# Kernel optimization log

Hardware: AMD Instinct MI355X
Metric: run time of the kernel (lower is better)

## Reference

```python
import jax, jax.numpy as jnp
import numpy as np

N, E = 50000, 800000
NODE_DIM, EDGE_DIM, HID = 128, 32, 128
NEG_SLOPE = 0.2


def _init(key, shape, fan_in):
    # glorot-ish init for weights
    return jax.random.normal(key, shape, dtype=jnp.float32) * (1.0 / np.sqrt(fan_in))


def setup_inputs() -> dict:
    key = jax.random.key(0)
    ks = jax.random.split(key, 20)
    x = jax.random.normal(ks[0], (N, NODE_DIM), dtype=jnp.float32)
    edge_index = jax.random.randint(ks[1], (2, E), 0, N, dtype=jnp.int64)
    edge_attr = jax.random.normal(ks[2], (E, EDGE_DIM), dtype=jnp.float32)
    params = {
        'W_emb': _init(ks[3], (NODE_DIM, HID), NODE_DIM),
        'b_emb': jnp.zeros((HID,), jnp.float32),
        # conv1 (GATv2Conv, heads=1)
        'Wl1': _init(ks[4], (HID, HID), HID), 'bl1': jnp.zeros((HID,), jnp.float32),
        'Wr1': _init(ks[5], (HID, HID), HID),
        'We1': _init(ks[6], (EDGE_DIM, HID), EDGE_DIM),
        'att1': _init(ks[7], (HID,), HID),
        'bo1': jnp.zeros((HID,), jnp.float32),
        # conv2
        'Wl2': _init(ks[8], (HID, HID), HID), 'bl2': jnp.zeros((HID,), jnp.float32),
        'Wr2': _init(ks[9], (HID, HID), HID),
        'We2': _init(ks[10], (EDGE_DIM, HID), EDGE_DIM),
        'att2': _init(ks[11], (HID,), HID),
        'bo2': jnp.zeros((HID,), jnp.float32),
    }
    return {'x': x, 'edge_index': edge_index, 'edge_attr': edge_attr, **params}


def _gatv2(x, src, dst, edge_attr, Wl, bl, Wr, We, att, bo, n_nodes):
    """PyG GATv2Conv (heads=1, add_self_loops=True, fill_value='mean')."""
    xl = x @ Wl + bl          # [N, H] source transform
    xr = x @ Wr               # [N, H] target transform
    # --- add self loops; self-loop edge_attr = mean of incoming edge_attr ---
    ones = jnp.ones((src.shape[0],), x.dtype)
    deg = jax.ops.segment_sum(ones, dst, num_segments=n_nodes)
    loop_attr = jax.ops.segment_sum(edge_attr, dst, num_segments=n_nodes) \
        / jnp.maximum(deg, 1.0)[:, None]
    loops = jnp.arange(n_nodes, dtype=src.dtype)
    src2 = jnp.concatenate([src, loops])
    dst2 = jnp.concatenate([dst, loops])
    ea2 = jnp.concatenate([edge_attr, loop_attr], axis=0)
    # --- per-edge attention (GATv2: leaky_relu AFTER the sum, score via att) ---
    xl_j = xl[src2]                                  # [E', H]
    msg = xl_j + xr[dst2] + ea2 @ We                 # [E', H]
    logits = jax.nn.leaky_relu(msg, NEG_SLOPE) @ att  # [E']
    # --- softmax over incoming edges per target node ---
    m = jax.ops.segment_max(logits, dst2, num_segments=n_nodes)
    ez = jnp.exp(logits - m[dst2])
    denom = jax.ops.segment_sum(ez, dst2, num_segments=n_nodes)
    alpha = ez / denom[dst2]                         # [E']
    # --- scatter-add aggregation ---
    out = jax.ops.segment_sum(alpha[:, None] * xl_j, dst2, num_segments=n_nodes)
    return out + bo


def reference(x, edge_index, edge_attr, W_emb, b_emb,
              Wl1, bl1, Wr1, We1, att1, bo1,
              Wl2, bl2, Wr2, We2, att2, bo2):
    src, dst = edge_index[0], edge_index[1]
    n = x.shape[0]
    h = x @ W_emb + b_emb
    h = jax.nn.silu(_gatv2(h, src, dst, edge_attr, Wl1, bl1, Wr1, We1, att1, bo1, n))
    h = jax.nn.silu(_gatv2(h, src, dst, edge_attr, Wl2, bl2, Wr2, We2, att2, bo2, n))
    return h
```

## Files before the change

### kernel.cpp

```cpp
#include <hip/hip_runtime.h>
#include <hip/hip_bf16.h>
#include <math.h>


#define HIP_N 50000
#define HIP_E 800000
#define HIP_H 128
#define HIP_ED 32
#define NEG_SLOPE 0.2f
#define RESCALE_THR_LOG2 11.5416f
#define LINM 3125
#define SCATB ((HIP_E + 255) / 256)
#define INV_LN2 1.4426950408889634f

typedef __fp16 h2 __attribute__((ext_vector_type(2)));
typedef _Float16 half8 __attribute__((ext_vector_type(8)));
typedef float f32x4 __attribute__((ext_vector_type(4)));

__device__ __forceinline__ h2 u2h(unsigned int u) {
    union { unsigned int u; h2 h; } c; c.u = u; return c.h;
}
__device__ __forceinline__ unsigned int pkh(float a, float b) {
    union { h2 h; unsigned int u; } c;
    c.h = __builtin_amdgcn_cvt_pkrtz(a, b);
    return c.u;
}
__device__ __forceinline__ float2 h2f(unsigned int u) {
    h2 h = u2h(u);
    return make_float2((float)h.x, (float)h.y);
}
__device__ __forceinline__ half8 u4h8(uint4 u) {
    union { uint4 u; half8 h; } c; c.u = u; return c.h;
}

__device__ __forceinline__ int fetch_idx(const int* __restrict__ ei, int is32, long long pos) {
    return is32 ? ei[pos] : ei[2 * pos];
}

__device__ __forceinline__ int wave_is32(const int* __restrict__ ei, int e) {
    int probe = (e < HIP_E) ? ei[2 * (long long)e + 1] : 0;
    return __any(probe != 0);
}

#define PREP_NB (420 + (HIP_N + 127) / 128)

__global__ __launch_bounds__(128) void k_prep(
    const float* __restrict__ Wemb, const float* __restrict__ bemb,
    const float* __restrict__ Wl1, const float* __restrict__ bl1,
    const float* __restrict__ Wr1,
    const float* __restrict__ Wl2, const float* __restrict__ bl2,
    const float* __restrict__ Wr2,
    const float* __restrict__ We1, const float* __restrict__ We2,
    unsigned short* __restrict__ Wt1, unsigned short* __restrict__ Wt2,
    float* __restrict__ b1, float* __restrict__ b2,
    unsigned int* __restrict__ Wepk1, unsigned int* __restrict__ Wepk2,
    int* __restrict__ deg) {
    int b = blockIdx.x, t = threadIdx.x;
    if (b < 256) {
        int r = b & 127;
        const float* W = (b < 128) ? Wl1 : Wr1;
        int nofs = (b < 128) ? 0 : 128;
        float acc = 0.f;
        for (int k = 0; k < 128; ++k) acc += Wemb[r * 128 + k] * W[k * 128 + t];
        union { __fp16 h; unsigned short s; } cv;
        cv.h = (__fp16)acc;
        Wt1[(size_t)(nofs + t) * 128 + r] = cv.s;
    } else if (b == 256) {
        float acc = bl1[t];
        for (int k = 0; k < 128; ++k) acc += bemb[k] * Wl1[k * 128 + t];
        b1[t] = acc;
    } else if (b == 257) {
        float acc = 0.f;
        for (int k = 0; k < 128; ++k) acc += bemb[k] * Wr1[k * 128 + t];
        b1[128 + t] = acc;
    } else if (b == 258) {
        b2[t] = bl2[t];
    } else if (b == 259) {
        b2[128 + t] = 0.f;
    } else if (b < 388) {
        int k = b - 260;
        float vl = Wl2[k * 128 + t], vr = Wr2[k * 128 + t];
        union { __fp16 h; unsigned short s; } c1, c2;
        c1.h = (__fp16)vl; c2.h = (__fp16)vr;
        Wt2[(size_t)t * 128 + k] = c1.s;
        Wt2[(size_t)(128 + t) * 128 + k] = c2.s;
    } else if (b < 420) {
        int idx = (b - 388) * 128 + t;
        const float* We = (idx < 2048) ? We1 : We2;
        unsigned int* P = (idx < 2048) ? Wepk1 : Wepk2;
        int r = idx & 2047;
        int d2 = r >> 7, rem = r & 127;
        int j = rem >> 6, tt = rem & 63;
        int col = 2 * tt + j;
        P[r] = pkh(We[(2 * d2) * 128 + col], We[(2 * d2 + 1) * 128 + col]);
    } else {
        int i = (b - 420) * 128 + t;
        if (i < HIP_N) deg[i] = 0;
    }
}

__global__ void k_hist(const int* __restrict__ ei, int* __restrict__ deg) {
    int e = blockIdx.x * blockDim.x + threadIdx.x;
    int is32 = wave_is32(ei, e);
    if (e < HIP_E) {
        int d = fetch_idx(ei, is32, (long long)HIP_E + e);
        atomicAdd(&deg[d], 1);
    }
}

#define SCAN_TILE 1024
#define SCAN_NB ((HIP_N + SCAN_TILE - 1) / SCAN_TILE)

__global__ __launch_bounds__(256) void k_scan1(const int* __restrict__ deg,
                                               int* __restrict__ bsums) {
    __shared__ int ws[4];
    int b = blockIdx.x, t = threadIdx.x;
    int base = b * SCAN_TILE;
    int v = 0;
#pragma unroll
    for (int j = 0; j < 4; ++j) {
        int i = base + t + 256 * j;
        if (i < HIP_N) v += deg[i];
    }
#pragma unroll
    for (int off = 32; off > 0; off >>= 1) v += __shfl_xor(v, off);
    int lane = t & 63, wid = t >> 6;
    if (lane == 0) ws[wid] = v;
    __syncthreads();
    if (t == 0) bsums[b] = ws[0] + ws[1] + ws[2] + ws[3];
}

__global__ __launch_bounds__(1024) void k_scan3(const int* __restrict__ deg,
                                                const int* __restrict__ bsums,
                                                int* __restrict__ offs,
                                                int* __restrict__ cursor) {
    __shared__ int wsum[16];
    __shared__ int bbase_sh;
    int b = blockIdx.x, t = threadIdx.x;
    int i = b * SCAN_TILE + t;
    int lane = t & 63, wid = t >> 6;
    if (wid == 0) {
        int v = (lane < SCAN_NB && lane < b) ? bsums[lane] : 0;
#pragma unroll
        for (int off = 32; off > 0; off >>= 1) v += __shfl_xor(v, off);
        if (lane == 0) bbase_sh = v;
    }
    int v = (i < HIP_N) ? deg[i] : 0;
    int incl = v;
#pragma unroll
    for (int off = 1; off < 64; off <<= 1) {
        int u = __shfl_up(incl, off);
        if (lane >= off) incl += u;
    }
    if (lane == 63) wsum[wid] = incl;
    __syncthreads();
    if (wid == 0 && lane < 16) {
        int w = wsum[lane];
#pragma unroll
        for (int off = 1; off < 16; off <<= 1) {
            int u = __shfl_up(w, off);
            if (lane >= off) w += u;
        }
        wsum[lane] = w;
    }
    __syncthreads();
    int baseadd = bbase_sh + (wid > 0 ? wsum[wid - 1] : 0);
    int excl = baseadd + incl - v;
    if (i < HIP_N) {
        offs[i] = excl;
        cursor[i] = excl;
        if (i == HIP_N - 1) offs[HIP_N] = excl + v;
    }
}

template <bool AHALF>
__device__ __forceinline__ void linm_body(const float* __restrict__ Af,
                                          const unsigned int* __restrict__ Ah,
                                          const unsigned short* __restrict__ Wt,
                                          const float* __restrict__ bias,
                                          unsigned int* __restrict__ xlh,
                                          unsigned int* __restrict__ xrh, int blk) {
    int tid = threadIdx.x;
    int wid = tid >> 6, l = tid & 63;
    int li = l & 15, lk = l >> 4;
    int rowA = blk * 16 + li;

    f32x4 acc0 = {0.f, 0.f, 0.f, 0.f};
    f32x4 acc1 = {0.f, 0.f, 0.f, 0.f};
    f32x4 acc2 = {0.f, 0.f, 0.f, 0.f};
    f32x4 acc3 = {0.f, 0.f, 0.f, 0.f};

#pragma unroll
    for (int ks = 0; ks < 4; ++ks) {
        int kb = ks * 32 + lk * 8;
        half8 afrag;
        if (AHALF) {
            afrag = u4h8(*(const uint4*)(Ah + (size_t)rowA * 64 + (kb >> 1)));
        } else {
            const float4* ap = (const float4*)(Af + (size_t)rowA * 128 + kb);
            float4 a0 = ap[0], a1 = ap[1];
            afrag = u4h8(make_uint4(pkh(a0.x, a0.y), pkh(a0.z, a0.w),
                                    pkh(a1.x, a1.y), pkh(a1.z, a1.w)));
        }
        int nbase = wid * 64 + li;
        half8 b0 = u4h8(*(const uint4*)(Wt + (size_t)(nbase +  0) * 128 + kb));
        half8 b1 = u4h8(*(const uint4*)(Wt + (size_t)(nbase + 16) * 128 + kb));
        half8 b2 = u4h8(*(const uint4*)(Wt + (size_t)(nbase + 32) * 128 + kb));
        half8 b3 = u4h8(*(const uint4*)(Wt + (size_t)(nbase + 48) * 128 + kb));
        acc0 = __builtin_amdgcn_mfma_f32_16x16x32_f16(afrag, b0, acc0, 0, 0, 0);
        acc1 = __builtin_amdgcn_mfma_f32_16x16x32_f16(afrag, b1, acc1, 0, 0, 0);
        acc2 = __builtin_amdgcn_mfma_f32_16x16x32_f16(afrag, b2, acc2, 0, 0, 0);
        acc3 = __builtin_amdgcn_mfma_f32_16x16x32_f16(afrag, b3, acc3, 0, 0, 0);
    }

    bool even = !(l & 1);
#pragma unroll
    for (int nt = 0; nt < 4; ++nt) {
        f32x4 a = (nt == 0) ? acc0 : (nt == 1) ? acc1 : (nt == 2) ? acc2 : acc3;
        int n = wid * 64 + nt * 16 + li;
        float bb = bias[n];
        unsigned int* outp = (n < 128) ? xlh : xrh;
        int nn = n & 127;
#pragma unroll
        for (int r = 0; r < 4; ++r) {
            int rowg = blk * 16 + lk * 4 + r;
            float v = a[r] + bb;
            float v1 = __shfl_down(v, 1);
            if (even) outp[(size_t)rowg * 64 + (nn >> 1)] = pkh(v, v1);
        }
    }
}

__device__ __forceinline__ void scatter_body(const int* __restrict__ ei, int is32,
                                             int* __restrict__ cursor,
                                             int* __restrict__ e_src,
                                             const float* __restrict__ ea,
                                             unsigned int* __restrict__ ea_h, int e) {
    if (e < HIP_E) {
        int s = fetch_idx(ei, is32, e);
        int d = fetch_idx(ei, is32, (long long)HIP_E + e);
        int pos = atomicAdd(&cursor[d], 1);
        e_src[pos] = s;
        const float4* src4 = (const float4*)(ea + (size_t)e * HIP_ED);
        float4 s0 = src4[0], s1 = src4[1], s2 = src4[2], s3 = src4[3];
        float4 s4 = src4[4], s5 = src4[5], s6 = src4[6], s7 = src4[7];
        uint4* dst = (uint4*)(ea_h + (size_t)pos * 16);
        dst[0] = make_uint4(pkh(s0.x, s0.y), pkh(s0.z, s0.w),
                            pkh(s1.x, s1.y), pkh(s1.z, s1.w));
        dst[1] = make_uint4(pkh(s2.x, s2.y), pkh(s2.z, s2.w),
                            pkh(s3.x, s3.y), pkh(s3.z, s3.w));
        dst[2] = make_uint4(pkh(s4.x, s4.y), pkh(s4.z, s4.w),
                            pkh(s5.x, s5.y), pkh(s5.z, s5.w));
        dst[3] = make_uint4(pkh(s6.x, s6.y), pkh(s6.z, s6.w),
                            pkh(s7.x, s7.y), pkh(s7.z, s7.w));
    }
}

__global__ __launch_bounds__(256) void k_fat1(
    const float* __restrict__ x, const unsigned short* __restrict__ Wt1,
    const float* __restrict__ b1,
    unsigned int* __restrict__ xlh, unsigned int* __restrict__ xrh,
    const int* __restrict__ ei,
    int* __restrict__ cursor, int* __restrict__ e_src,
    const float* __restrict__ ea, unsigned int* __restrict__ ea_h) {
    if (blockIdx.x < LINM) {
        linm_body<false>(x, nullptr, Wt1, b1, xlh, xrh, blockIdx.x);
    } else {
        int e = (blockIdx.x - LINM) * 256 + threadIdx.x;
        int is32 = wave_is32(ei, e);
        scatter_body(ei, is32, cursor, e_src, ea, ea_h, e);
    }
}

__global__ __launch_bounds__(256) void k_linm(const unsigned int* __restrict__ hh,
                                              const unsigned short* __restrict__ Wt,
                                              const float* __restrict__ bias,
                                              unsigned int* __restrict__ xlh,
                                              unsigned int* __restrict__ xrh) {
    linm_body<true>(nullptr, hh, Wt, bias, xlh, xrh, blockIdx.x);
}

template <int OUTH>
__global__ __launch_bounds__(64) void k_node_fused(
    const int* __restrict__ offs, const int* __restrict__ e_src,
    const unsigned int* __restrict__ ea_h,
    const unsigned int* __restrict__ Wepk, const float* __restrict__ att,
    const unsigned int* __restrict__ xlh, const unsigned int* __restrict__ xrh,
    const float* __restrict__ bo,
    unsigned int* __restrict__ houth, float* __restrict__ houtf) {
    int i = blockIdx.x;
    int t = threadIdx.x;

    h2 wx00 = u2h(Wepk[ 0*128 + t]),      wy00 = u2h(Wepk[ 0*128 + 64 + t]);
    h2 wx01 = u2h(Wepk[ 1*128 + t]),      wy01 = u2h(Wepk[ 1*128 + 64 + t]);
    h2 wx02 = u2h(Wepk[ 2*128 + t]),      wy02 = u2h(Wepk[ 2*128 + 64 + t]);
    h2 wx03 = u2h(Wepk[ 3*128 + t]),      wy03 = u2h(Wepk[ 3*128 + 64 + t]);
    h2 wx04 = u2h(Wepk[ 4*128 + t]),      wy04 = u2h(Wepk[ 4*128 + 64 + t]);
    h2 wx05 = u2h(Wepk[ 5*128 + t]),      wy05 = u2h(Wepk[ 5*128 + 64 + t]);
    h2 wx06 = u2h(Wepk[ 6*128 + t]),      wy06 = u2h(Wepk[ 6*128 + 64 + t]);
    h2 wx07 = u2h(Wepk[ 7*128 + t]),      wy07 = u2h(Wepk[ 7*128 + 64 + t]);
    h2 wx08 = u2h(Wepk[ 8*128 + t]),      wy08 = u2h(Wepk[ 8*128 + 64 + t]);
    h2 wx09 = u2h(Wepk[ 9*128 + t]),      wy09 = u2h(Wepk[ 9*128 + 64 + t]);
    h2 wx10 = u2h(Wepk[10*128 + t]),      wy10 = u2h(Wepk[10*128 + 64 + t]);
    h2 wx11 = u2h(Wepk[11*128 + t]),      wy11 = u2h(Wepk[11*128 + 64 + t]);
    h2 wx12 = u2h(Wepk[12*128 + t]),      wy12 = u2h(Wepk[12*128 + 64 + t]);
    h2 wx13 = u2h(Wepk[13*128 + t]),      wy13 = u2h(Wepk[13*128 + 64 + t]);
    h2 wx14 = u2h(Wepk[14*128 + t]),      wy14 = u2h(Wepk[14*128 + 64 + t]);
    h2 wx15 = u2h(Wepk[15*128 + t]),      wy15 = u2h(Wepk[15*128 + 64 + t]);

    float2 attv = ((const float2*)att)[t];
    attv.x *= INV_LN2; attv.y *= INV_LN2;
    float2 bov  = ((const float2*)bo)[t];
    float2 xri  = h2f(xrh[(size_t)i * 64 + t]);
    float2 xli  = h2f(xlh[(size_t)i * 64 + t]);

    float m = -1e30f;
    float denom = 0.f;
    float accx = 0.f, accy = 0.f;
    float epsx = 0.f, epsy = 0.f;

    int o0 = offs[i], o1 = offs[i + 1];
    int cnt = o1 - o0;
    int pairs = cnt >> 1;

#define DOTP(EX, EY, U, K)                                            \
    EX = __builtin_amdgcn_fdot2(u2h(U), wx##K, EX, false);            \
    EY = __builtin_amdgcn_fdot2(u2h(U), wy##K, EY, false);

#define EPROJ(EX, EY, P)                                              \
    {                                                                 \
        uint4 q0 = ((const uint4*)(P))[0];                            \
        uint4 q1 = ((const uint4*)(P))[1];                            \
        uint4 q2 = ((const uint4*)(P))[2];                            \
        uint4 q3 = ((const uint4*)(P))[3];                            \
        DOTP(EX, EY, q0.x, 00) DOTP(EX, EY, q0.y, 01)                 \
        DOTP(EX, EY, q0.z, 02) DOTP(EX, EY, q0.w, 03)                 \
        DOTP(EX, EY, q1.x, 04) DOTP(EX, EY, q1.y, 05)                 \
        DOTP(EX, EY, q1.z, 06) DOTP(EX, EY, q1.w, 07)                 \
        DOTP(EX, EY, q2.x, 08) DOTP(EX, EY, q2.y, 09)                 \
        DOTP(EX, EY, q2.z, 10) DOTP(EX, EY, q2.w, 11)                 \
        DOTP(EX, EY, q3.x, 12) DOTP(EX, EY, q3.y, 13)                 \
        DOTP(EX, EY, q3.z, 14) DOTP(EX, EY, q3.w, 15)                 \
    }

    unsigned int uA = 0, uB = 0;
    if (pairs > 0) {
        int s0 = e_src[o0];
        int s1 = e_src[o0 + 1];
        uA = xlh[(size_t)s0 * 64 + t];
        uB = xlh[(size_t)s1 * 64 + t];
    }

    for (int pp = 0; pp < pairs; ++pp) {
        int e = o0 + 2 * pp;
        float2 x0 = h2f(uA), x1 = h2f(uB);
        if (pp + 1 < pairs) {
            int s0 = e_src[e + 2];
            int s1 = e_src[e + 3];
            uA = xlh[(size_t)s0 * 64 + t];
            uB = xlh[(size_t)s1 * 64 + t];
        }
        const unsigned int* er = ea_h + (size_t)e * 16;
        float ex0 = 0.f, ey0 = 0.f, ex1 = 0.f, ey1 = 0.f;
        EPROJ(ex0, ey0, er)
        EPROJ(ex1, ey1, er + 16)
        epsx += ex0 + ex1; epsy += ey0 + ey1;
        float vx0 = x0.x + xri.x + ex0, vy0 = x0.y + xri.y + ey0;
        float vx1 = x1.x + xri.x + ex1, vy1 = x1.y + xri.y + ey1;
        vx0 = fmaxf(vx0, NEG_SLOPE * vx0);
        vy0 = fmaxf(vy0, NEG_SLOPE * vy0);
        vx1 = fmaxf(vx1, NEG_SLOPE * vx1);
        vy1 = fmaxf(vy1, NEG_SLOPE * vy1);
        float p0 = vx0 * attv.x + vy0 * attv.y;
        float p1 = vx1 * attv.x + vy1 * attv.y;
#pragma unroll
        for (int off = 32; off > 0; off >>= 1) {
            p0 += __shfl_xor(p0, off);
            p1 += __shfl_xor(p1, off);
        }
        float pm = fmaxf(p0, p1);
        if (pm > m + RESCALE_THR_LOG2) {
            float sc = exp2f(m - pm);
            accx *= sc; accy *= sc; denom *= sc;
            m = pm;
        }
        float wA = exp2f(p0 - m);
        float wB = exp2f(p1 - m);
        accx += wA * x0.x + wB * x1.x;
        accy += wA * x0.y + wB * x1.y;
        denom += wA + wB;
    }

    if (cnt & 1) {
        int e = o1 - 1;
        int s = e_src[e];
        float2 x0 = h2f(xlh[(size_t)s * 64 + t]);
        const unsigned int* er = ea_h + (size_t)e * 16;
        float ex = 0.f, ey = 0.f;
        EPROJ(ex, ey, er)
        epsx += ex; epsy += ey;
        float vx = x0.x + xri.x + ex;
        float vy = x0.y + xri.y + ey;
        vx = fmaxf(vx, NEG_SLOPE * vx);
        vy = fmaxf(vy, NEG_SLOPE * vy);
        float p = vx * attv.x + vy * attv.y;
#pragma unroll
        for (int off = 32; off > 0; off >>= 1) p += __shfl_xor(p, off);
        if (p > m + RESCALE_THR_LOG2) {
            float sc = exp2f(m - p);
            accx *= sc; accy *= sc; denom *= sc;
            m = p;
        }
        float w = exp2f(p - m);
        accx += w * x0.x;
        accy += w * x0.y;
        denom += w;
    }
#undef EPROJ
#undef DOTP

    float invdeg = 1.f / fmaxf((float)cnt, 1.f);
    float sx = xli.x + xri.x + epsx * invdeg;
    float sy = xli.y + xri.y + epsy * invdeg;
    sx = fmaxf(sx, NEG_SLOPE * sx);
    sy = fmaxf(sy, NEG_SLOPE * sy);
    float ps = sx * attv.x + sy * attv.y;
#pragma unroll
    for (int off = 32; off > 0; off >>= 1) ps += __shfl_xor(ps, off);

    float mm = fmaxf(m, ps);
    float wf = exp2f(m - mm);
    float ws = exp2f(ps - mm);
    denom = denom * wf + ws;
    accx = accx * wf + ws * xli.x;
    accy = accy * wf + ws * xli.y;

    float ox = accx / denom + bov.x;
    float oy = accy / denom + bov.y;
    float sox = ox / (1.f + __expf(-ox));
    float soy = oy / (1.f + __expf(-oy));
    if (OUTH) {
        houth[(size_t)i * 64 + t] = pkh(sox, soy);
    } else {
        float2 o; o.x = sox; o.y = soy;
        ((float2*)(houtf + (size_t)i * HIP_H))[t] = o;
    }
}

extern "C" void kernel_launch(void* const* d_in, const int* in_sizes, int n_in,
                              void* d_out, int out_size, void* d_ws, size_t ws_size,
                              hipStream_t stream) {
    const float* x      = (const float*)d_in[0];
    const int*   ei     = (const int*)d_in[1];
    const float* ea     = (const float*)d_in[2];
    const float* W_emb  = (const float*)d_in[3];
    const float* b_emb  = (const float*)d_in[4];
    const float* Wl1    = (const float*)d_in[5];
    const float* bl1    = (const float*)d_in[6];
    const float* Wr1    = (const float*)d_in[7];
    const float* We1    = (const float*)d_in[8];
    const float* att1   = (const float*)d_in[9];
    const float* bo1    = (const float*)d_in[10];
    const float* Wl2    = (const float*)d_in[11];
    const float* bl2    = (const float*)d_in[12];
    const float* Wr2    = (const float*)d_in[13];
    const float* We2    = (const float*)d_in[14];
    const float* att2   = (const float*)d_in[15];
    const float* bo2    = (const float*)d_in[16];
    float* out = (float*)d_out;

    char* p = (char*)d_ws;
    auto carve = [&](size_t bytes) {
        void* q = (void*)p;
        p += (bytes + 255) / 256 * 256;
        return q;
    };
    unsigned int* hh  = (unsigned int*)carve((size_t)HIP_N * 64 * 4);
    unsigned int* xlh = (unsigned int*)carve((size_t)HIP_N * 64 * 4);
    unsigned int* xrh = (unsigned int*)carve((size_t)HIP_N * 64 * 4);
    unsigned int* ea_h = (unsigned int*)carve((size_t)HIP_E * 16 * 4);
    int*   deg      = (int*)carve((size_t)HIP_N * 4);
    int*   offs     = (int*)carve((size_t)(HIP_N + 1) * 4);
    int*   cursor   = (int*)carve((size_t)HIP_N * 4);
    int*   e_src    = (int*)carve((size_t)HIP_E * 4);
    int*   bsums    = (int*)carve((size_t)SCAN_NB * 4);
    unsigned int* Wepk1 = (unsigned int*)carve(2048 * 4);
    unsigned int* Wepk2 = (unsigned int*)carve(2048 * 4);
    unsigned short* Wt1 = (unsigned short*)carve(256 * 128 * 2);
    unsigned short* Wt2 = (unsigned short*)carve(256 * 128 * 2);
    float* b1       = (float*)carve(256 * 4);
    float* b2       = (float*)carve(256 * 4);

    k_prep<<<PREP_NB, 128, 0, stream>>>(W_emb, b_emb, Wl1, bl1, Wr1,
                                        Wl2, bl2, Wr2, We1, We2,
                                        Wt1, Wt2, b1, b2,
                                        Wepk1, Wepk2, deg);

    k_hist<<<(HIP_E + 255) / 256, 256, 0, stream>>>(ei, deg);
    k_scan1<<<SCAN_NB, 256, 0, stream>>>(deg, bsums);
    k_scan3<<<SCAN_NB, 1024, 0, stream>>>(deg, bsums, offs, cursor);

    k_fat1<<<LINM + SCATB, 256, 0, stream>>>(x, Wt1, b1, xlh, xrh,
                                             ei, cursor, e_src, ea, ea_h);

    k_node_fused<1><<<HIP_N, 64, 0, stream>>>(offs, e_src, ea_h, Wepk1, att1,
                                              xlh, xrh, bo1, hh, nullptr);
    k_linm<<<LINM, 256, 0, stream>>>(hh, Wt2, b2, xlh, xrh);
    k_node_fused<0><<<HIP_N, 64, 0, stream>>>(offs, e_src, ea_h, Wepk2, att2,
                                              xlh, xrh, bo2, nullptr, out);
}
```

Baseline: 436.5 us.

## Compute per-edge attribute projection with MFMA in node attention kernel

The per-node attention kernel now processes 16 incoming edges per iteration and computes the edge-attribute projection with 16x16x32 f16 MFMA instructions instead of per-lane fdot2 chains. The hidden feature layout is permuted so each lane owns 8 interleaved channels; the linear kernels' epilogues, the layer-2 weight packing and the att/bias vectors are reordered to match. This targets the ALU-bound edge projection and widens gathers to 16-byte loads. The cost is padding waste for low-degree nodes, extra cross-lane reductions, and a more fragile layout contract between kernels.

```diff
diff --git a/kernel.cpp b/kernel.cpp
--- a/kernel.cpp
+++ b/kernel.cpp
@@ -25,10 +25,8 @@
     c.h = __builtin_amdgcn_cvt_pkrtz(a, b);
     return c.u;
 }
-__device__ __forceinline__ float2 h2f(unsigned int u) {
-    h2 h = u2h(u);
-    return make_float2((float)h.x, (float)h.y);
-}
+__device__ __forceinline__ float hlo(unsigned int u) { return (float)u2h(u).x; }
+__device__ __forceinline__ float hhi(unsigned int u) { return (float)u2h(u).y; }
 __device__ __forceinline__ half8 u4h8(uint4 u) {
     union { uint4 u; half8 h; } c; c.u = u; return c.h;
 }
@@ -42,7 +40,7 @@
     return __any(probe != 0);
 }
 
-#define PREP_NB (420 + (HIP_N + 127) / 128)
+#define PREP_NB (400 + (HIP_N + 127) / 128)
 
 __global__ __launch_bounds__(128) void k_prep(
     const float* __restrict__ Wemb, const float* __restrict__ bemb,
@@ -51,9 +49,13 @@
     const float* __restrict__ Wl2, const float* __restrict__ bl2,
     const float* __restrict__ Wr2,
     const float* __restrict__ We1, const float* __restrict__ We2,
+    const float* __restrict__ att1, const float* __restrict__ bo1,
+    const float* __restrict__ att2, const float* __restrict__ bo2,
     unsigned short* __restrict__ Wt1, unsigned short* __restrict__ Wt2,
     float* __restrict__ b1, float* __restrict__ b2,
-    unsigned int* __restrict__ Wepk1, unsigned int* __restrict__ Wepk2,
+    uint4* __restrict__ WemB1, uint4* __restrict__ WemB2,
+    float* __restrict__ attp1, float* __restrict__ bop1,
+    float* __restrict__ attp2, float* __restrict__ bop2,
     int* __restrict__ deg) {
     int b = blockIdx.x, t = threadIdx.x;
     if (b < 256) {
@@ -78,23 +80,36 @@
     } else if (b == 259) {
         b2[128 + t] = 0.f;
     } else if (b < 388) {
-        int k = b - 260;
-        float vl = Wl2[k * 128 + t], vr = Wr2[k * 128 + t];
+        int pk = b - 260;
+        int d = (pk >> 3) + ((pk & 7) << 4);
+        float vl = Wl2[d * 128 + t], vr = Wr2[d * 128 + t];
         union { __fp16 h; unsigned short s; } c1, c2;
         c1.h = (__fp16)vl; c2.h = (__fp16)vr;
-        Wt2[(size_t)t * 128 + k] = c1.s;
-        Wt2[(size_t)(128 + t) * 128 + k] = c2.s;
-    } else if (b < 420) {
+        Wt2[(size_t)t * 128 + pk] = c1.s;
+        Wt2[(size_t)(128 + t) * 128 + pk] = c2.s;
+    } else if (b < 396) {
         int idx = (b - 388) * 128 + t;
-        const float* We = (idx < 2048) ? We1 : We2;
-        unsigned int* P = (idx < 2048) ? Wepk1 : Wepk2;
-        int r = idx & 2047;
-        int d2 = r >> 7, rem = r & 127;
-        int j = rem >> 6, tt = rem & 63;
-        int col = 2 * tt + j;
-        P[r] = pkh(We[(2 * d2) * 128 + col], We[(2 * d2 + 1) * 128 + col]);
+        int layer = idx >> 9, rem = idx & 511;
+        int n = rem >> 6, ll = rem & 63;
+        int col = 16 * n + (ll & 15);
+        int kb = (ll >> 4) * 8;
+        const float* We = layer ? We2 : We1;
+        uint4 v = make_uint4(
+            pkh(We[(kb + 0) * 128 + col], We[(kb + 1) * 128 + col]),
+            pkh(We[(kb + 2) * 128 + col], We[(kb + 3) * 128 + col]),
+            pkh(We[(kb + 4) * 128 + col], We[(kb + 5) * 128 + col]),
+            pkh(We[(kb + 6) * 128 + col], We[(kb + 7) * 128 + col]));
+        (layer ? WemB2 : WemB1)[rem] = v;
+    } else if (b < 400) {
+        int which = b - 396;
+        int li = t >> 3, q = t & 7;
+        int src = li + 16 * q;
+        if (which == 0)      attp1[t] = att1[src] * INV_LN2;
+        else if (which == 1) bop1[t]  = bo1[src];
+        else if (which == 2) attp2[t] = att2[src] * INV_LN2;
+        else                 bop2[t]  = bo2[src];
     } else {
-        int i = (b - 420) * 128 + t;
+        int i = (b - 400) * 128 + t;
         if (i < HIP_N) deg[i] = 0;
     }
 }
@@ -213,21 +228,21 @@
         acc3 = __builtin_amdgcn_mfma_f32_16x16x32_f16(afrag, b3, acc3, 0, 0, 0);
     }
 
-    bool even = !(l & 1);
-#pragma unroll
-    for (int nt = 0; nt < 4; ++nt) {
-        f32x4 a = (nt == 0) ? acc0 : (nt == 1) ? acc1 : (nt == 2) ? acc2 : acc3;
-        int n = wid * 64 + nt * 16 + li;
-        float bb = bias[n];
-        unsigned int* outp = (n < 128) ? xlh : xrh;
-        int nn = n & 127;
-#pragma unroll
-        for (int r = 0; r < 4; ++r) {
-            int rowg = blk * 16 + lk * 4 + r;
-            float v = a[r] + bb;
-            float v1 = __shfl_down(v, 1);
-            if (even) outp[(size_t)rowg * 64 + (nn >> 1)] = pkh(v, v1);
-        }
+    unsigned int* outp = (wid < 2) ? xlh : xrh;
+    int wsel = wid & 1;
+    float bb0 = bias[wid * 64 +  0 + li];
+    float bb1 = bias[wid * 64 + 16 + li];
+    float bb2 = bias[wid * 64 + 32 + li];
+    float bb3 = bias[wid * 64 + 48 + li];
+#pragma unroll
+    for (int r = 0; r < 4; ++r) {
+        int rowg = blk * 16 + lk * 4 + r;
+        float v0 = acc0[r] + bb0;
+        float v1 = acc1[r] + bb1;
+        float v2 = acc2[r] + bb2;
+        float v3 = acc3[r] + bb3;
+        uint2 st = make_uint2(pkh(v0, v1), pkh(v2, v3));
+        *(uint2*)(outp + (size_t)rowg * 64 + li * 4 + wsel * 2) = st;
     }
 }
 
@@ -281,169 +296,174 @@
 }
 
 template <int OUTH>
-__global__ __launch_bounds__(64) void k_node_fused(
+__global__ __launch_bounds__(64) void k_node_mfma(
     const int* __restrict__ offs, const int* __restrict__ e_src,
     const unsigned int* __restrict__ ea_h,
-    const unsigned int* __restrict__ Wepk, const float* __restrict__ att,
+    const uint4* __restrict__ WemB, const float* __restrict__ att_p,
     const unsigned int* __restrict__ xlh, const unsigned int* __restrict__ xrh,
-    const float* __restrict__ bo,
+    const float* __restrict__ bo_p,
     unsigned int* __restrict__ houth, float* __restrict__ houtf) {
     int i = blockIdx.x;
-    int t = threadIdx.x;
-
-    h2 wx00 = u2h(Wepk[ 0*128 + t]),      wy00 = u2h(Wepk[ 0*128 + 64 + t]);
-    h2 wx01 = u2h(Wepk[ 1*128 + t]),      wy01 = u2h(Wepk[ 1*128 + 64 + t]);
-    h2 wx02 = u2h(Wepk[ 2*128 + t]),      wy02 = u2h(Wepk[ 2*128 + 64 + t]);
-    h2 wx03 = u2h(Wepk[ 3*128 + t]),      wy03 = u2h(Wepk[ 3*128 + 64 + t]);
-    h2 wx04 = u2h(Wepk[ 4*128 + t]),      wy04 = u2h(Wepk[ 4*128 + 64 + t]);
-    h2 wx05 = u2h(Wepk[ 5*128 + t]),      wy05 = u2h(Wepk[ 5*128 + 64 + t]);
-    h2 wx06 = u2h(Wepk[ 6*128 + t]),      wy06 = u2h(Wepk[ 6*128 + 64 + t]);
-    h2 wx07 = u2h(Wepk[ 7*128 + t]),      wy07 = u2h(Wepk[ 7*128 + 64 + t]);
-    h2 wx08 = u2h(Wepk[ 8*128 + t]),      wy08 = u2h(Wepk[ 8*128 + 64 + t]);
-    h2 wx09 = u2h(Wepk[ 9*128 + t]),      wy09 = u2h(Wepk[ 9*128 + 64 + t]);
-    h2 wx10 = u2h(Wepk[10*128 + t]),      wy10 = u2h(Wepk[10*128 + 64 + t]);
-    h2 wx11 = u2h(Wepk[11*128 + t]),      wy11 = u2h(Wepk[11*128 + 64 + t]);
-    h2 wx12 = u2h(Wepk[12*128 + t]),      wy12 = u2h(Wepk[12*128 + 64 + t]);
-    h2 wx13 = u2h(Wepk[13*128 + t]),      wy13 = u2h(Wepk[13*128 + 64 + t]);
-    h2 wx14 = u2h(Wepk[14*128 + t]),      wy14 = u2h(Wepk[14*128 + 64 + t]);
-    h2 wx15 = u2h(Wepk[15*128 + t]),      wy15 = u2h(Wepk[15*128 + 64 + t]);
-
-    float2 attv = ((const float2*)att)[t];
-    attv.x *= INV_LN2; attv.y *= INV_LN2;
-    float2 bov  = ((const float2*)bo)[t];
-    float2 xri  = h2f(xrh[(size_t)i * 64 + t]);
-    float2 xli  = h2f(xlh[(size_t)i * 64 + t]);
-
-    float m = -1e30f;
-    float denom = 0.f;
-    float accx = 0.f, accy = 0.f;
-    float epsx = 0.f, epsy = 0.f;
+    int l = threadIdx.x, li = l & 15, lk = l >> 4;
+
+    float attv[8], xriv[8];
+    {
+        const float4* ap = (const float4*)(att_p + li * 8);
+        float4 q0 = ap[0], q1 = ap[1];
+        attv[0]=q0.x; attv[1]=q0.y; attv[2]=q0.z; attv[3]=q0.w;
+        attv[4]=q1.x; attv[5]=q1.y; attv[6]=q1.z; attv[7]=q1.w;
+        uint4 xr4 = *(const uint4*)(xrh + (size_t)i * 64 + li * 4);
+        xriv[0]=hlo(xr4.x); xriv[1]=hhi(xr4.x); xriv[2]=hlo(xr4.y); xriv[3]=hhi(xr4.y);
+        xriv[4]=hlo(xr4.z); xriv[5]=hhi(xr4.z); xriv[6]=hlo(xr4.w); xriv[7]=hhi(xr4.w);
+    }
 
     int o0 = offs[i], o1 = offs[i + 1];
     int cnt = o1 - o0;
-    int pairs = cnt >> 1;
-
-#define DOTP(EX, EY, U, K)                                            \
-    EX = __builtin_amdgcn_fdot2(u2h(U), wx##K, EX, false);            \
-    EY = __builtin_amdgcn_fdot2(u2h(U), wy##K, EY, false);
-
-#define EPROJ(EX, EY, P)                                              \
-    {                                                                 \
-        uint4 q0 = ((const uint4*)(P))[0];                            \
-        uint4 q1 = ((const uint4*)(P))[1];                            \
-        uint4 q2 = ((const uint4*)(P))[2];                            \
-        uint4 q3 = ((const uint4*)(P))[3];                            \
-        DOTP(EX, EY, q0.x, 00) DOTP(EX, EY, q0.y, 01)                 \
-        DOTP(EX, EY, q0.z, 02) DOTP(EX, EY, q0.w, 03)                 \
-        DOTP(EX, EY, q1.x, 04) DOTP(EX, EY, q1.y, 05)                 \
-        DOTP(EX, EY, q1.z, 06) DOTP(EX, EY, q1.w, 07)                 \
-        DOTP(EX, EY, q2.x, 08) DOTP(EX, EY, q2.y, 09)                 \
-        DOTP(EX, EY, q2.z, 10) DOTP(EX, EY, q2.w, 11)                 \
-        DOTP(EX, EY, q3.x, 12) DOTP(EX, EY, q3.y, 13)                 \
-        DOTP(EX, EY, q3.z, 14) DOTP(EX, EY, q3.w, 15)                 \
-    }
-
-    unsigned int uA = 0, uB = 0;
-    if (pairs > 0) {
-        int s0 = e_src[o0];
-        int s1 = e_src[o0 + 1];
-        uA = xlh[(size_t)s0 * 64 + t];
-        uB = xlh[(size_t)s1 * 64 + t];
-    }
-
-    for (int pp = 0; pp < pairs; ++pp) {
-        int e = o0 + 2 * pp;
-        float2 x0 = h2f(uA), x1 = h2f(uB);
-        if (pp + 1 < pairs) {
-            int s0 = e_src[e + 2];
-            int s1 = e_src[e + 3];
-            uA = xlh[(size_t)s0 * 64 + t];
-            uB = xlh[(size_t)s1 * 64 + t];
-        }
-        const unsigned int* er = ea_h + (size_t)e * 16;
-        float ex0 = 0.f, ey0 = 0.f, ex1 = 0.f, ey1 = 0.f;
-        EPROJ(ex0, ey0, er)
-        EPROJ(ex1, ey1, er + 16)
-        epsx += ex0 + ex1; epsy += ey0 + ey1;
-        float vx0 = x0.x + xri.x + ex0, vy0 = x0.y + xri.y + ey0;
-        float vx1 = x1.x + xri.x + ex1, vy1 = x1.y + xri.y + ey1;
-        vx0 = fmaxf(vx0, NEG_SLOPE * vx0);
-        vy0 = fmaxf(vy0, NEG_SLOPE * vy0);
-        vx1 = fmaxf(vx1, NEG_SLOPE * vx1);
-        vy1 = fmaxf(vy1, NEG_SLOPE * vy1);
-        float p0 = vx0 * attv.x + vy0 * attv.y;
-        float p1 = vx1 * attv.x + vy1 * attv.y;
-#pragma unroll
-        for (int off = 32; off > 0; off >>= 1) {
-            p0 += __shfl_xor(p0, off);
-            p1 += __shfl_xor(p1, off);
-        }
-        float pm = fmaxf(p0, p1);
+
+    float m = -1e30f, denom = 0.f;
+    float acc[8] = {0,0,0,0,0,0,0,0};
+    float eps[8] = {0,0,0,0,0,0,0,0};
+
+    for (int base = o0; base < o1; base += 16) {
+        int ea_e = base + li;
+        uint4 au = (ea_e < o1) ? *(const uint4*)(ea_h + (size_t)ea_e * 16 + lk * 4)
+                               : make_uint4(0, 0, 0, 0);
+        half8 afrag = u4h8(au);
+
+        int sv[4]; int val[4]; uint4 xlu[4];
+#pragma unroll
+        for (int r = 0; r < 4; ++r) {
+            int idx = base + lk * 4 + r;
+            val[r] = idx < o1;
+            sv[r] = val[r] ? e_src[idx] : 0;
+        }
+#pragma unroll
+        for (int r = 0; r < 4; ++r)
+            xlu[r] = *(const uint4*)(xlh + (size_t)sv[r] * 64 + li * 4);
+
+        float p[4] = {0.f, 0.f, 0.f, 0.f};
+#pragma unroll
+        for (int pass = 0; pass < 2; ++pass) {
+            const uint4* wb = WemB + pass * 256 + l;
+            half8 bf0 = u4h8(wb[0]);
+            half8 bf1 = u4h8(wb[64]);
+            half8 bf2 = u4h8(wb[128]);
+            half8 bf3 = u4h8(wb[192]);
+            f32x4 c0 = {0,0,0,0}, c1 = {0,0,0,0}, c2 = {0,0,0,0}, c3 = {0,0,0,0};
+            c0 = __builtin_amdgcn_mfma_f32_16x16x32_f16(afrag, bf0, c0, 0, 0, 0);
+            c1 = __builtin_amdgcn_mfma_f32_16x16x32_f16(afrag, bf1, c1, 0, 0, 0);
+            c2 = __builtin_amdgcn_mfma_f32_16x16x32_f16(afrag, bf2, c2, 0, 0, 0);
+            c3 = __builtin_amdgcn_mfma_f32_16x16x32_f16(afrag, bf3, c3, 0, 0, 0);
+#pragma unroll
+            for (int nn = 0; nn < 4; ++nn) {
+                int n = pass * 4 + nn;
+                f32x4 C = (nn == 0) ? c0 : (nn == 1) ? c1 : (nn == 2) ? c2 : c3;
+                float av = attv[n], xr_ = xriv[n];
+#pragma unroll
+                for (int r = 0; r < 4; ++r) {
+                    unsigned int dw = ((const unsigned int*)&xlu[r])[n >> 1];
+                    float xv = (n & 1) ? hhi(dw) : hlo(dw);
+                    float v = xv + xr_ + C[r];
+                    v = fmaxf(v, NEG_SLOPE * v);
+                    p[r] += v * av;
+                }
+                eps[n] += C[0] + C[1] + C[2] + C[3];
+            }
+        }
+#pragma unroll
+        for (int off = 1; off <= 8; off <<= 1) {
+            p[0] += __shfl_xor(p[0], off);
+            p[1] += __shfl_xor(p[1], off);
+            p[2] += __shfl_xor(p[2], off);
+            p[3] += __shfl_xor(p[3], off);
+        }
+#pragma unroll
+        for (int r = 0; r < 4; ++r) if (!val[r]) p[r] = -1e30f;
+        float pm = fmaxf(fmaxf(p[0], p[1]), fmaxf(p[2], p[3]));
+        pm = fmaxf(pm, __shfl_xor(pm, 16));
+        pm = fmaxf(pm, __shfl_xor(pm, 32));
         if (pm > m + RESCALE_THR_LOG2) {
             float sc = exp2f(m - pm);
-            accx *= sc; accy *= sc; denom *= sc;
+#pragma unroll
+            for (int q = 0; q < 8; ++q) acc[q] *= sc;
+            denom *= sc;
             m = pm;
         }
-        float wA = exp2f(p0 - m);
-        float wB = exp2f(p1 - m);
-        accx += wA * x0.x + wB * x1.x;
-        accy += wA * x0.y + wB * x1.y;
-        denom += wA + wB;
-    }
-
-    if (cnt & 1) {
-        int e = o1 - 1;
-        int s = e_src[e];
-        float2 x0 = h2f(xlh[(size_t)s * 64 + t]);
-        const unsigned int* er = ea_h + (size_t)e * 16;
-        float ex = 0.f, ey = 0.f;
-        EPROJ(ex, ey, er)
-        epsx += ex; epsy += ey;
-        float vx = x0.x + xri.x + ex;
-        float vy = x0.y + xri.y + ey;
-        vx = fmaxf(vx, NEG_SLOPE * vx);
-        vy = fmaxf(vy, NEG_SLOPE * vy);
-        float p = vx * attv.x + vy * attv.y;
-#pragma unroll
-        for (int off = 32; off > 0; off >>= 1) p += __shfl_xor(p, off);
-        if (p > m + RESCALE_THR_LOG2) {
-            float sc = exp2f(m - p);
-            accx *= sc; accy *= sc; denom *= sc;
-            m = p;
-        }
-        float w = exp2f(p - m);
-        accx += w * x0.x;
-        accy += w * x0.y;
-        denom += w;
-    }
-#undef EPROJ
-#undef DOTP
-
+        float w0 = exp2f(p[0] - m);
+        float w1 = exp2f(p[1] - m);
+        float w2 = exp2f(p[2] - m);
+        float w3 = exp2f(p[3] - m);
+        denom += w0 + w1 + w2 + w3;
+#pragma unroll
+        for (int q = 0; q < 8; ++q) {
+            unsigned int d0 = ((const unsigned int*)&xlu[0])[q >> 1];
+            unsigned int d1 = ((const unsigned int*)&xlu[1])[q >> 1];
+            unsigned int d2 = ((const unsigned int*)&xlu[2])[q >> 1];
+            unsigned int d3 = ((const unsigned int*)&xlu[3])[q >> 1];
+            float x0 = (q & 1) ? hhi(d0) : hlo(d0);
+            float x1 = (q & 1) ? hhi(d1) : hlo(d1);
+            float x2 = (q & 1) ? hhi(d2) : hlo(d2);
+            float x3 = (q & 1) ? hhi(d3) : hlo(d3);
+            acc[q] += w0 * x0 + w1 * x1 + w2 * x2 + w3 * x3;
+        }
+    }
+
+#pragma unroll
+    for (int off = 16; off <= 32; off <<= 1) {
+#pragma unroll
+        for (int q = 0; q < 8; ++q) {
+            acc[q] += __shfl_xor(acc[q], off);
+            eps[q] += __shfl_xor(eps[q], off);
+        }
+        denom += __shfl_xor(denom, off);
+    }
+
+    float xliv[8];
+    {
+        uint4 xl4 = *(const uint4*)(xlh + (size_t)i * 64 + li * 4);
+        xliv[0]=hlo(xl4.x); xliv[1]=hhi(xl4.x); xliv[2]=hlo(xl4.y); xliv[3]=hhi(xl4.y);
+        xliv[4]=hlo(xl4.z); xliv[5]=hhi(xl4.z); xliv[6]=hlo(xl4.w); xliv[7]=hhi(xl4.w);
+    }
     float invdeg = 1.f / fmaxf((float)cnt, 1.f);
-    float sx = xli.x + xri.x + epsx * invdeg;
-    float sy = xli.y + xri.y + epsy * invdeg;
-    sx = fmaxf(sx, NEG_SLOPE * sx);
-    sy = fmaxf(sy, NEG_SLOPE * sy);
-    float ps = sx * attv.x + sy * attv.y;
-#pragma unroll
-    for (int off = 32; off > 0; off >>= 1) ps += __shfl_xor(ps, off);
+    float ps = 0.f;
+#pragma unroll
+    for (int q = 0; q < 8; ++q) {
+        float sv = xliv[q] + xriv[q] + eps[q] * invdeg;
+        sv = fmaxf(sv, NEG_SLOPE * sv);
+        ps += sv * attv[q];
+    }
+#pragma unroll
+    for (int off = 1; off <= 8; off <<= 1) ps += __shfl_xor(ps, off);
 
     float mm = fmaxf(m, ps);
     float wf = exp2f(m - mm);
     float ws = exp2f(ps - mm);
     denom = denom * wf + ws;
-    accx = accx * wf + ws * xli.x;
-    accy = accy * wf + ws * xli.y;
-
-    float ox = accx / denom + bov.x;
-    float oy = accy / denom + bov.y;
-    float sox = ox / (1.f + __expf(-ox));
-    float soy = oy / (1.f + __expf(-oy));
-    if (OUTH) {
-        houth[(size_t)i * 64 + t] = pkh(sox, soy);
-    } else {
-        float2 o; o.x = sox; o.y = soy;
-        ((float2*)(houtf + (size_t)i * HIP_H))[t] = o;
+
+    float bov[8];
+    {
+        const float4* bp = (const float4*)(bo_p + li * 8);
+        float4 q0 = bp[0], q1 = bp[1];
+        bov[0]=q0.x; bov[1]=q0.y; bov[2]=q0.z; bov[3]=q0.w;
+        bov[4]=q1.x; bov[5]=q1.y; bov[6]=q1.z; bov[7]=q1.w;
+    }
+    float o[8];
+#pragma unroll
+    for (int q = 0; q < 8; ++q) {
+        float a = acc[q] * wf + ws * xliv[q];
+        float ox = a / denom + bov[q];
+        o[q] = ox / (1.f + __expf(-ox));
+    }
+    if (lk == 0) {
+        if (OUTH) {
+            uint4 st = make_uint4(pkh(o[0], o[1]), pkh(o[2], o[3]),
+                                  pkh(o[4], o[5]), pkh(o[6], o[7]));
+            *(uint4*)(houth + (size_t)i * 64 + li * 4) = st;
+        } else {
+#pragma unroll
+            for (int n = 0; n < 8; ++n)
+                houtf[(size_t)i * 128 + li + 16 * n] = o[n];
+        }
     }
 }
 
@@ -484,17 +504,23 @@
     int*   cursor   = (int*)carve((size_t)HIP_N * 4);
     int*   e_src    = (int*)carve((size_t)HIP_E * 4);
     int*   bsums    = (int*)carve((size_t)SCAN_NB * 4);
-    unsigned int* Wepk1 = (unsigned int*)carve(2048 * 4);
-    unsigned int* Wepk2 = (unsigned int*)carve(2048 * 4);
     unsigned short* Wt1 = (unsigned short*)carve(256 * 128 * 2);
     unsigned short* Wt2 = (unsigned short*)carve(256 * 128 * 2);
     float* b1       = (float*)carve(256 * 4);
     float* b2       = (float*)carve(256 * 4);
+    uint4* WemB1    = (uint4*)carve(512 * 16);
+    uint4* WemB2    = (uint4*)carve(512 * 16);
+    float* attp1    = (float*)carve(128 * 4);
+    float* bop1     = (float*)carve(128 * 4);
+    float* attp2    = (float*)carve(128 * 4);
+    float* bop2     = (float*)carve(128 * 4);
 
     k_prep<<<PREP_NB, 128, 0, stream>>>(W_emb, b_emb, Wl1, bl1, Wr1,
                                         Wl2, bl2, Wr2, We1, We2,
+                                        att1, bo1, att2, bo2,
                                         Wt1, Wt2, b1, b2,
-                                        Wepk1, Wepk2, deg);
+                                        WemB1, WemB2, attp1, bop1, attp2, bop2,
+                                        deg);
 
     k_hist<<<(HIP_E + 255) / 256, 256, 0, stream>>>(ei, deg);
     k_scan1<<<SCAN_NB, 256, 0, stream>>>(deg, bsums);
@@ -503,9 +529,9 @@
     k_fat1<<<LINM + SCATB, 256, 0, stream>>>(x, Wt1, b1, xlh, xrh,
                                              ei, cursor, e_src, ea, ea_h);
 
-    k_node_fused<1><<<HIP_N, 64, 0, stream>>>(offs, e_src, ea_h, Wepk1, att1,
-                                              xlh, xrh, bo1, hh, nullptr);
+    k_node_mfma<1><<<HIP_N, 64, 0, stream>>>(offs, e_src, ea_h, WemB1, attp1,
+                                             xlh, xrh, bop1, hh, nullptr);
     k_linm<<<LINM, 256, 0, stream>>>(hh, Wt2, b2, xlh, xrh);
-    k_node_fused<0><<<HIP_N, 64, 0, stream>>>(offs, e_src, ea_h, Wepk2, att2,
-                                              xlh, xrh, bo2, nullptr, out);
-}
+    k_node_mfma<0><<<HIP_N, 64, 0, stream>>>(offs, e_src, ea_h, WemB2, attp2,
+                                             xlh, xrh, bop2, nullptr, out);
+}
```

After: 445.0 us. No clear change (+1.9%).
